# Kernel tuning notes

Hardware: AMD Instinct MI355X
Metric: run time of the kernel (lower is better)

## Reference

```python
import jax, jax.numpy as jnp
import numpy as np

CH = 256
CQK = CH // 8
B, H, W = 4, 64, 64


def setup_inputs() -> dict:
    key = jax.random.key(0)
    ks = jax.random.split(key, 8)
    s_qk = 1.0 / np.sqrt(CH)  # MSR init for 1x1 conv: std = 1/sqrt(fan_in)
    x = jax.random.normal(ks[0], (B, CH, H, W), dtype=jnp.float32)
    Wq = jax.random.normal(ks[1], (CQK, CH), dtype=jnp.float32) * s_qk
    bq = jnp.zeros((CQK,), dtype=jnp.float32)
    Wk = jax.random.normal(ks[2], (CQK, CH), dtype=jnp.float32) * s_qk
    bk = jnp.zeros((CQK,), dtype=jnp.float32)
    Wv = jax.random.normal(ks[3], (CH, CH), dtype=jnp.float32) * s_qk
    bv = jnp.zeros((CH,), dtype=jnp.float32)
    # NOTE: module inits gamma=0; use a nonzero value so the attention branch is active
    gamma = jnp.float32(0.5) * jnp.ones((1,), dtype=jnp.float32)
    return {"x": x, "Wq": Wq, "bq": bq, "Wk": Wk, "bk": bk, "Wv": Wv, "bv": bv, "gamma": gamma}


def reference(x, Wq, bq, Wk, bk, Wv, bv, gamma):
    b, c, h, w = x.shape
    n = h * w
    xf = x.reshape(b, c, n)  # [B, C, N]
    # 1x1 convs are per-pixel channel projections
    q = jnp.einsum('oc,bcn->bon', Wq, xf) + bq[:, None]  # [B, C/8, N]
    k = jnp.einsum('oc,bcn->bon', Wk, xf) + bk[:, None]  # [B, C/8, N]
    v = jnp.einsum('oc,bcn->bon', Wv, xf) + bv[:, None]  # [B, C, N]
    # scores[b, i, j] = q[:, i] . k[:, j]  (no scaling, as in source)
    att = jax.nn.softmax(jnp.einsum('bci,bcj->bij', q, k), axis=-1)  # [B, N, N]
    out = jnp.einsum('bcj,bij->bci', v, att).reshape(b, c, h, w)
    return x + gamma[0] * out
```

## Files before the change

### kernel.cpp

```cpp
#include <hip/hip_runtime.h>
#include <hip/hip_bf16.h>

typedef unsigned short u16;
typedef __attribute__((ext_vector_type(8))) __bf16 bf16x8;
typedef __attribute__((ext_vector_type(8))) unsigned short u16x8;
typedef __attribute__((ext_vector_type(4))) float f32x4;
typedef __attribute__((ext_vector_type(16))) float f32x16;
typedef __attribute__((ext_vector_type(4))) unsigned int u32x4;
typedef __attribute__((ext_vector_type(2))) unsigned int u32x2;

#define MFMA16(a, b, c) __builtin_amdgcn_mfma_f32_16x16x32_bf16((a), (b), (c), 0, 0, 0)
#define MFMA32(a, b, c) __builtin_amdgcn_mfma_f32_32x32x16_bf16((a), (b), (c), 0, 0, 0)

#define BN 4
#define CH 256
#define CQK 32
#define NPIX 4096

__device__ __forceinline__ u16 f2bf(float f) {
    __hip_bfloat16 h = __float2bfloat16(f);
    return *reinterpret_cast<u16*>(&h);
}

__device__ __forceinline__ unsigned pack2(float a, float b) {
    return (unsigned)f2bf(a) | ((unsigned)f2bf(b) << 16);
}

__device__ __forceinline__ unsigned packtr(float a, float b) {
    return (__float_as_uint(b) & 0xffff0000u) | (__float_as_uint(a) >> 16);
}

__device__ __forceinline__ float bf2f(u16 v) {
    return __uint_as_float(((unsigned)v) << 16);
}

__device__ __forceinline__ f32x16 zero16() {
    f32x16 z;
#pragma unroll
    for (int i = 0; i < 16; ++i) z[i] = 0.f;
    return z;
}

__device__ __forceinline__ int perm16(int k) {
    return (k & 3) | ((k & 4) << 1) | ((k & 8) >> 1);
}

__global__ void k_transpose(const float* __restrict__ x, u16* __restrict__ xt) {
    __shared__ float xs[64][65];
    int n0 = blockIdx.x * 64, c0 = blockIdx.y * 64, b = blockIdx.z;
    int t = threadIdx.x;
    const float* xp = x + ((size_t)(b * CH + c0)) * NPIX + n0;
#pragma unroll
    for (int it = 0; it < 16; ++it) {
        int idx = it * 256 + t;
        int cc = idx >> 6, nn = idx & 63;
        xs[cc][nn] = xp[(size_t)cc * NPIX + nn];
    }
    __syncthreads();
    u16* op = xt + ((size_t)(b * NPIX + n0)) * CH + c0;
#pragma unroll
    for (int it = 0; it < 16; ++it) {
        int idx = it * 256 + t;
        int nn = idx >> 6, cc = idx & 63;
        op[(size_t)nn * CH + cc] = f2bf(xs[cc][nn]);
    }
}

__global__ void k_wcvt(const float* __restrict__ Wq, const float* __restrict__ Wk,
                       const float* __restrict__ Wv, u16* __restrict__ Wbf) {
    int idx = blockIdx.x * 256 + threadIdx.x;
    int o = idx >> 8, c = idx & 255;
    float v;
    if (o < 32) v = Wq[o * 256 + c];
    else if (o < 64) v = Wk[(o - 32) * 256 + c];
    else v = Wv[(o - 64) * 256 + c];
    Wbf[idx] = f2bf(v);
}

__launch_bounds__(256, 1)
__global__ void k_proj(const u16* __restrict__ Wbf, const u16* __restrict__ xt,
                       const float* __restrict__ bq, const float* __restrict__ bk,
                       const float* __restrict__ bv,
                       u16* __restrict__ qb, u16* __restrict__ kb, u16* __restrict__ vb) {
    int b = blockIdx.y, n0 = blockIdx.x * 64;
    int t = threadIdx.x, w = t >> 6, l = t & 63;
    int lr = l & 15, lg = l >> 4;

    f32x4 acc[5][4];
#pragma unroll
    for (int s = 0; s < 5; ++s)
#pragma unroll
        for (int u = 0; u < 4; ++u) acc[s][u] = f32x4{0.f, 0.f, 0.f, 0.f};

    const u16* xtb = xt + ((size_t)(b * NPIX + n0)) * CH;

#pragma unroll
    for (int kk = 0; kk < 8; ++kk) {
        int kof = kk * 32 + lg * 8;
        bf16x8 af[5], bfr[4];
#pragma unroll
        for (int s = 0; s < 5; ++s) {
            int o = w * 16 + s * 64 + lr;
            af[s] = *reinterpret_cast<const bf16x8*>(Wbf + (size_t)o * 256 + kof);
        }
#pragma unroll
        for (int u = 0; u < 4; ++u) {
            int n = u * 16 + lr;
            bfr[u] = *reinterpret_cast<const bf16x8*>(xtb + (size_t)n * CH + kof);
        }
#pragma unroll
        for (int s = 0; s < 5; ++s)
#pragma unroll
            for (int u = 0; u < 4; ++u) acc[s][u] = MFMA16(af[s], bfr[u], acc[s][u]);
    }

    int lrp = perm16(lr);
#pragma unroll
    for (int s = 0; s < 5; ++s) {
        int o0 = w * 16 + s * 64;
#pragma unroll
        for (int r = 0; r < 4; ++r) {
            int o = o0 + lg * 4 + r;
            float bias = (o < 32) ? bq[o] : (o < 64) ? bk[o - 32] : bv[o - 64];
#pragma unroll
            for (int u = 0; u < 4; ++u) {
                float val = acc[s][u][r] + bias;
                u16 h = f2bf(val);
                if (o < 32) qb[((size_t)b * NPIX + n0 + u * 16 + lr) * CQK + o] = h;
                else if (o < 64) kb[((size_t)b * NPIX + n0 + u * 16 + lr) * CQK + (o - 32)] = h;
                else vb[((size_t)(b * CH + (o - 64))) * NPIX + n0 + u * 16 + lrp] = h;
            }
        }
    }
}

template <int NCHUNK>
__launch_bounds__(256, 2)
__global__ void k_attn5(const u16* __restrict__ qb, const u16* __restrict__ kb,
                        const u16* __restrict__ vb, const float* __restrict__ x,
                        const float* __restrict__ gamma,
                        u16* __restrict__ pacc, float* __restrict__ plsum,
                        float* __restrict__ out) {
    constexpr int JCH = NPIX / NCHUNK;
    constexpr int NT = JCH / 32;
    int it = blockIdx.x, s = blockIdx.y, b = blockIdx.z;
    int t = threadIdx.x, w = t >> 6, l = t & 63;
    int lr = l & 31, hi = l >> 5;
    int i0 = it * 128;
    int j0 = s * JCH;

    __shared__ u16 vlds[3][256][32];
    __shared__ float lsl[128];

    const u16* qrow = qb + ((size_t)b * NPIX + i0 + w * 32 + lr) * CQK;
    bf16x8 qf0 = *(const bf16x8*)(qrow + hi * 8);
    bf16x8 qf1 = *(const bf16x8*)(qrow + 16 + hi * 8);

    const u16* kbase = kb + (size_t)b * NPIX * CQK;
    const u16* vbase = vb + (size_t)(b * CH) * NPIX;

    f32x16 acc[8];
#pragma unroll
    for (int ct = 0; ct < 8; ++ct) acc[ct] = zero16();
    float lsum_p = 0.f;

    int srow = t >> 2, sslot = t & 3;
    int wslot = (sslot ^ (srow & 3)) * 8;
    bf16x8 vst[4];
    bf16x8 kc0, kc1;

    auto vload = [&](int tt) {
#pragma unroll
        for (int m = 0; m < 4; ++m)
            vst[m] = *(const bf16x8*)(vbase + (size_t)(64 * m + srow) * NPIX +
                                      j0 + tt * 32 + sslot * 8);
    };
    auto vwrite = [&](int buf) {
        u16* base = &vlds[buf][0][0];
#pragma unroll
        for (int m = 0; m < 4; ++m)
            *(bf16x8*)(base + (64 * m + srow) * 32 + wslot) = vst[m];
    };
    auto kload = [&](int tt) {
        const u16* kr = kbase + (size_t)(j0 + tt * 32 + lr) * CQK;
        kc0 = *(const bf16x8*)(kr + hi * 8);
        kc1 = *(const bf16x8*)(kr + 16 + hi * 8);
    };
    auto qkexp = [&](bf16x8 k0, bf16x8 k1, bf16x8& p0, bf16x8& p1) {
        f32x16 sf = MFMA32(k0, qf0, zero16());
        sf = MFMA32(k1, qf1, sf);
        float P[16];
#pragma unroll
        for (int e = 0; e < 16; ++e) {
            P[e] = __expf(sf[e] - 32.0f);
            lsum_p += P[e];
        }
        u32x4 a = {packtr(P[0], P[1]), packtr(P[2], P[3]),
                   packtr(P[4], P[5]), packtr(P[6], P[7])};
        u32x4 c = {packtr(P[8], P[9]), packtr(P[10], P[11]),
                   packtr(P[12], P[13]), packtr(P[14], P[15])};
        p0 = __builtin_bit_cast(bf16x8, a);
        p1 = __builtin_bit_cast(bf16x8, c);
    };
    auto pv = [&](int buf, bf16x8 p0, bf16x8 p1) {
        const u16* base = &vlds[buf][0][0];
#pragma unroll
        for (int ct = 0; ct < 8; ++ct) {
            int c = ct * 32 + lr;
            int sw = lr & 3;
            bf16x8 vf0 = *(const bf16x8*)(base + c * 32 + ((hi ^ sw) * 8));
            bf16x8 vf1 = *(const bf16x8*)(base + c * 32 + (((2 + hi) ^ sw) * 8));
            acc[ct] = MFMA32(p0, vf0, acc[ct]);
            acc[ct] = MFMA32(p1, vf1, acc[ct]);
        }
    };
    auto lds_barrier = [&]() {
        asm volatile("s_waitcnt lgkmcnt(0)" ::: "memory");
        __builtin_amdgcn_s_barrier();
    };

    bf16x8 paA0, paA1, paB0, paB1;
    vload(0);
    kload(0);
    vwrite(0);
    vload(1);
    lds_barrier();
    qkexp(kc0, kc1, paA0, paA1);
    if (1 < NT) kload(1);
    vwrite(1);
    if (2 < NT) vload(2);

    int bR = 0, bW = 2;
    for (int tt = 0; tt < NT; ++tt) {
        if (tt + 1 < NT) qkexp(kc0, kc1, paB0, paB1);
        if (tt + 2 < NT) kload(tt + 2);
        pv(bR, paA0, paA1);
        if (tt + 2 < NT) vwrite(bW);
        if (tt + 3 < NT) vload(tt + 3);
        lds_barrier();
        if (tt + 1 < NT) { paA0 = paB0; paA1 = paB1; }
        bR = (bR == 2) ? 0 : bR + 1;
        bW = (bW == 2) ? 0 : bW + 1;
    }

    lsum_p += __shfl_xor(lsum_p, 32);

    if constexpr (NCHUNK == 1) {
        float g = gamma[0];
        if (l < 32) lsl[w * 32 + l] = g / lsum_p;
        __syncthreads();
#pragma unroll
        for (int ct = 0; ct < 8; ++ct) {
            int c = ct * 32 + lr;
            const float* xp = x + ((size_t)(b * CH + c)) * NPIX + i0;
            float* op = out + ((size_t)(b * CH + c)) * NPIX + i0;
#pragma unroll
            for (int r = 0; r < 16; ++r) {
                int il = w * 32 + (r & 3) + 8 * (r >> 2) + 4 * hi;
                op[il] = xp[il] + acc[ct][r] * lsl[il];
            }
        }
    } else {
        size_t pbase = ((((size_t)s * BN + b) * 32 + it) * 256) * 128;
#pragma unroll
        for (int ct = 0; ct < 8; ++ct) {
            int c = ct * 32 + lr;
#pragma unroll
            for (int q = 0; q < 4; ++q) {
                int il0 = w * 32 + 8 * q + 4 * hi;
                u32x2 pr = {pack2(acc[ct][4 * q], acc[ct][4 * q + 1]),
                            pack2(acc[ct][4 * q + 2], acc[ct][4 * q + 3])};
                *(u32x2*)(pacc + pbase + (size_t)c * 128 + il0) = pr;
            }
        }
        if (l < 32)
            plsum[(((size_t)s * BN + b) * 32 + it) * 128 + w * 32 + l] = lsum_p;
    }
}

template <int NCHUNK>
__global__ void k_reduce(const u16* __restrict__ pacc, const float* __restrict__ plsum,
                         const float* __restrict__ x, const float* __restrict__ gamma,
                         float* __restrict__ out) {
    int cg = blockIdx.x, it = blockIdx.y, b = blockIdx.z;
    int t = threadIdx.x;
    int c0 = cg * 32;
    __shared__ float invl[128];

    if (t < 128) {
        float lt = 0.f;
#pragma unroll
        for (int s = 0; s < NCHUNK; ++s)
            lt += plsum[(((size_t)s * BN + b) * 32 + it) * 128 + t];
        invl[t] = gamma[0] / lt;
    }
    __syncthreads();

    const size_t chunk_stride = (size_t)BN * 32 * 256 * 128;
    size_t base = (((size_t)b * 32 + it) * 256 + c0) * 128;

#pragma unroll
    for (int k = 0; k < 2; ++k) {
        int v = k * 256 + t;
        int cl = v >> 4;
        int io = (v & 15) * 8;
        size_t off = base + (size_t)cl * 128 + io;
        f32x4 a0 = {0.f, 0.f, 0.f, 0.f}, a1 = a0;
#pragma unroll
        for (int s = 0; s < NCHUNK; ++s) {
            u16x8 p = *(const u16x8*)(pacc + (size_t)s * chunk_stride + off);
            a0[0] += bf2f(p[0]); a0[1] += bf2f(p[1]); a0[2] += bf2f(p[2]); a0[3] += bf2f(p[3]);
            a1[0] += bf2f(p[4]); a1[1] += bf2f(p[5]); a1[2] += bf2f(p[6]); a1[3] += bf2f(p[7]);
        }
        f32x4 i0v = *(const f32x4*)(&invl[io]);
        f32x4 i1v = *(const f32x4*)(&invl[io + 4]);
        size_t oi = ((size_t)(b * CH + c0 + cl)) * NPIX + it * 128 + io;
        f32x4 x0 = *(const f32x4*)(x + oi);
        f32x4 x1 = *(const f32x4*)(x + oi + 4);
        *(f32x4*)(out + oi) = x0 + a0 * i0v;
        *(f32x4*)(out + oi + 4) = x1 + a1 * i1v;
    }
}

extern "C" void kernel_launch(void* const* d_in, const int* in_sizes, int n_in,
                              void* d_out, int out_size, void* d_ws, size_t ws_size,
                              hipStream_t stream) {
    const float* x = (const float*)d_in[0];
    const float* Wq = (const float*)d_in[1];
    const float* bq = (const float*)d_in[2];
    const float* Wk = (const float*)d_in[3];
    const float* bk = (const float*)d_in[4];
    const float* Wv = (const float*)d_in[5];
    const float* bv = (const float*)d_in[6];
    const float* gamma = (const float*)d_in[7];
    float* out = (float*)d_out;

    char* ws = (char*)d_ws;
    u16* xt = (u16*)(ws);
    u16* Wbf = (u16*)(ws + 8388608);
    u16* qb = (u16*)(ws + 8388608 + 163840);
    u16* kb = (u16*)(ws + 8388608 + 163840 + 1048576);
    u16* vb = (u16*)(ws + 8388608 + 163840 + 2097152);
    const size_t base_end = 8388608 + 163840 + 2097152 + 8388608;
    u16* pacc = (u16*)(ws + base_end);

    hipLaunchKernelGGL(k_transpose, dim3(64, 4, 4), dim3(256), 0, stream, x, xt);
    hipLaunchKernelGGL(k_wcvt, dim3(320), dim3(256), 0, stream, Wq, Wk, Wv, Wbf);
    hipLaunchKernelGGL(k_proj, dim3(64, 4), dim3(256), 0, stream, Wbf, xt, bq, bk, bv, qb, kb, vb);

    const size_t pacc4 = (size_t)4 * BN * NPIX * CH * 2;
    const size_t pls4 = (size_t)4 * BN * NPIX * 4;
    const size_t pacc2 = pacc4 / 2, pls2 = pls4 / 2;

    if (ws_size >= base_end + pacc4 + pls4) {
        float* plsum = (float*)(ws + base_end + pacc4);
        hipLaunchKernelGGL(k_attn5<4>, dim3(32, 4, 4), dim3(256), 0, stream,
                           qb, kb, vb, x, gamma, pacc, plsum, out);
        hipLaunchKernelGGL(k_reduce<4>, dim3(8, 32, 4), dim3(256), 0, stream,
                           pacc, plsum, x, gamma, out);
    } else if (ws_size >= base_end + pacc2 + pls2) {
        float* plsum = (float*)(ws + base_end + pacc2);
        hipLaunchKernelGGL(k_attn5<2>, dim3(32, 2, 4), dim3(256), 0, stream,
                           qb, kb, vb, x, gamma, pacc, plsum, out);
        hipLaunchKernelGGL(k_reduce<2>, dim3(8, 32, 4), dim3(256), 0, stream,
                           pacc, plsum, x, gamma, out);
    } else {
        hipLaunchKernelGGL(k_attn5<1>, dim3(32, 1, 4), dim3(256), 0, stream,
                           qb, kb, vb, x, gamma, pacc, (float*)pacc, out);
    }
}
```

Measured before the change: 93.25 us.

## Split attention work across 8 waves by query and channel quarters

```diff
diff --git a/kernel.cpp b/kernel.cpp
--- a/kernel.cpp
+++ b/kernel.cpp
@@ -135,8 +135,8 @@
 }
 
 template <int NCHUNK>
-__launch_bounds__(256, 2)
-__global__ void k_attn5(const u16* __restrict__ qb, const u16* __restrict__ kb,
+__launch_bounds__(512, 2)
+__global__ void k_attn6(const u16* __restrict__ qb, const u16* __restrict__ kb,
                         const u16* __restrict__ vb, const float* __restrict__ x,
                         const float* __restrict__ gamma,
                         u16* __restrict__ pacc, float* __restrict__ plsum,
@@ -146,72 +146,85 @@
     int it = blockIdx.x, s = blockIdx.y, b = blockIdx.z;
     int t = threadIdx.x, w = t >> 6, l = t & 63;
     int lr = l & 31, hi = l >> 5;
+    int iq2 = w >> 2, ch4 = w & 3;
     int i0 = it * 128;
     int j0 = s * JCH;
 
     __shared__ u16 vlds[3][256][32];
     __shared__ float lsl[128];
 
-    const u16* qrow = qb + ((size_t)b * NPIX + i0 + w * 32 + lr) * CQK;
-    bf16x8 qf0 = *(const bf16x8*)(qrow + hi * 8);
-    bf16x8 qf1 = *(const bf16x8*)(qrow + 16 + hi * 8);
+    bf16x8 qf[2][2];
+#pragma unroll
+    for (int is = 0; is < 2; ++is) {
+        const u16* qrow = qb + ((size_t)b * NPIX + i0 + iq2 * 64 + is * 32 + lr) * CQK;
+        qf[is][0] = *(const bf16x8*)(qrow + hi * 8);
+        qf[is][1] = *(const bf16x8*)(qrow + 16 + hi * 8);
+    }
 
     const u16* kbase = kb + (size_t)b * NPIX * CQK;
     const u16* vbase = vb + (size_t)(b * CH) * NPIX;
 
-    f32x16 acc[8];
-#pragma unroll
-    for (int ct = 0; ct < 8; ++ct) acc[ct] = zero16();
-    float lsum_p = 0.f;
-
-    int srow = t >> 2, sslot = t & 3;
-    int wslot = (sslot ^ (srow & 3)) * 8;
-    bf16x8 vst[4];
+    f32x16 acc[2][2];
+#pragma unroll
+    for (int is = 0; is < 2; ++is)
+#pragma unroll
+        for (int ct = 0; ct < 2; ++ct) acc[is][ct] = zero16();
+    float lsum[2] = {0.f, 0.f};
+
+    int row0 = t >> 2, sslot = t & 3;
+    int wso = (sslot ^ (row0 & 3)) * 8;
+    bf16x8 vst[2];
     bf16x8 kc0, kc1;
 
     auto vload = [&](int tt) {
 #pragma unroll
-        for (int m = 0; m < 4; ++m)
-            vst[m] = *(const bf16x8*)(vbase + (size_t)(64 * m + srow) * NPIX +
+        for (int m = 0; m < 2; ++m)
+            vst[m] = *(const bf16x8*)(vbase + (size_t)(row0 + 128 * m) * NPIX +
                                       j0 + tt * 32 + sslot * 8);
     };
     auto vwrite = [&](int buf) {
         u16* base = &vlds[buf][0][0];
 #pragma unroll
-        for (int m = 0; m < 4; ++m)
-            *(bf16x8*)(base + (64 * m + srow) * 32 + wslot) = vst[m];
+        for (int m = 0; m < 2; ++m)
+            *(bf16x8*)(base + (row0 + 128 * m) * 32 + wso) = vst[m];
     };
     auto kload = [&](int tt) {
         const u16* kr = kbase + (size_t)(j0 + tt * 32 + lr) * CQK;
         kc0 = *(const bf16x8*)(kr + hi * 8);
         kc1 = *(const bf16x8*)(kr + 16 + hi * 8);
     };
-    auto qkexp = [&](bf16x8 k0, bf16x8 k1, bf16x8& p0, bf16x8& p1) {
-        f32x16 sf = MFMA32(k0, qf0, zero16());
-        sf = MFMA32(k1, qf1, sf);
-        float P[16];
-#pragma unroll
-        for (int e = 0; e < 16; ++e) {
-            P[e] = __expf(sf[e] - 32.0f);
-            lsum_p += P[e];
-        }
-        u32x4 a = {packtr(P[0], P[1]), packtr(P[2], P[3]),
-                   packtr(P[4], P[5]), packtr(P[6], P[7])};
-        u32x4 c = {packtr(P[8], P[9]), packtr(P[10], P[11]),
-                   packtr(P[12], P[13]), packtr(P[14], P[15])};
-        p0 = __builtin_bit_cast(bf16x8, a);
-        p1 = __builtin_bit_cast(bf16x8, c);
-    };
-    auto pv = [&](int buf, bf16x8 p0, bf16x8 p1) {
+    auto qkexp = [&](bf16x8 k0, bf16x8 k1, bf16x8 (&pa)[4]) {
+#pragma unroll
+        for (int is = 0; is < 2; ++is) {
+            f32x16 sf = MFMA32(k0, qf[is][0], zero16());
+            sf = MFMA32(k1, qf[is][1], sf);
+            float P[16];
+#pragma unroll
+            for (int e = 0; e < 16; ++e) {
+                P[e] = __expf(sf[e] - 32.0f);
+                lsum[is] += P[e];
+            }
+            u32x4 a = {packtr(P[0], P[1]), packtr(P[2], P[3]),
+                       packtr(P[4], P[5]), packtr(P[6], P[7])};
+            u32x4 c = {packtr(P[8], P[9]), packtr(P[10], P[11]),
+                       packtr(P[12], P[13]), packtr(P[14], P[15])};
+            pa[is * 2] = __builtin_bit_cast(bf16x8, a);
+            pa[is * 2 + 1] = __builtin_bit_cast(bf16x8, c);
+        }
+    };
+    auto pv = [&](int buf, bf16x8 (&pa)[4]) {
         const u16* base = &vlds[buf][0][0];
 #pragma unroll
-        for (int ct = 0; ct < 8; ++ct) {
-            int c = ct * 32 + lr;
-            int sw = lr & 3;
+        for (int ct = 0; ct < 2; ++ct) {
+            int c = ch4 * 64 + ct * 32 + lr;
+            int sw = c & 3;
             bf16x8 vf0 = *(const bf16x8*)(base + c * 32 + ((hi ^ sw) * 8));
             bf16x8 vf1 = *(const bf16x8*)(base + c * 32 + (((2 + hi) ^ sw) * 8));
-            acc[ct] = MFMA32(p0, vf0, acc[ct]);
-            acc[ct] = MFMA32(p1, vf1, acc[ct]);
+#pragma unroll
+            for (int is = 0; is < 2; ++is) {
+                acc[is][ct] = MFMA32(pa[is * 2], vf0, acc[is][ct]);
+                acc[is][ct] = MFMA32(pa[is * 2 + 1], vf1, acc[is][ct]);
+            }
         }
     };
     auto lds_barrier = [&]() {
@@ -219,62 +232,76 @@
         __builtin_amdgcn_s_barrier();
     };
 
-    bf16x8 paA0, paA1, paB0, paB1;
+    bf16x8 paA[4], paB[4];
     vload(0);
     kload(0);
     vwrite(0);
     vload(1);
     lds_barrier();
-    qkexp(kc0, kc1, paA0, paA1);
+    qkexp(kc0, kc1, paA);
     if (1 < NT) kload(1);
     vwrite(1);
     if (2 < NT) vload(2);
 
     int bR = 0, bW = 2;
     for (int tt = 0; tt < NT; ++tt) {
-        if (tt + 1 < NT) qkexp(kc0, kc1, paB0, paB1);
+        if (tt + 1 < NT) qkexp(kc0, kc1, paB);
         if (tt + 2 < NT) kload(tt + 2);
-        pv(bR, paA0, paA1);
+        pv(bR, paA);
         if (tt + 2 < NT) vwrite(bW);
         if (tt + 3 < NT) vload(tt + 3);
         lds_barrier();
-        if (tt + 1 < NT) { paA0 = paB0; paA1 = paB1; }
+        if (tt + 1 < NT) {
+#pragma unroll
+            for (int e = 0; e < 4; ++e) paA[e] = paB[e];
+        }
         bR = (bR == 2) ? 0 : bR + 1;
         bW = (bW == 2) ? 0 : bW + 1;
     }
 
-    lsum_p += __shfl_xor(lsum_p, 32);
+    lsum[0] += __shfl_xor(lsum[0], 32);
+    lsum[1] += __shfl_xor(lsum[1], 32);
 
     if constexpr (NCHUNK == 1) {
         float g = gamma[0];
-        if (l < 32) lsl[w * 32 + l] = g / lsum_p;
+        if (ch4 == 0 && l < 32) {
+            lsl[iq2 * 64 + l] = g / lsum[0];
+            lsl[iq2 * 64 + 32 + l] = g / lsum[1];
+        }
         __syncthreads();
 #pragma unroll
-        for (int ct = 0; ct < 8; ++ct) {
-            int c = ct * 32 + lr;
-            const float* xp = x + ((size_t)(b * CH + c)) * NPIX + i0;
-            float* op = out + ((size_t)(b * CH + c)) * NPIX + i0;
-#pragma unroll
-            for (int r = 0; r < 16; ++r) {
-                int il = w * 32 + (r & 3) + 8 * (r >> 2) + 4 * hi;
-                op[il] = xp[il] + acc[ct][r] * lsl[il];
-            }
-        }
+        for (int is = 0; is < 2; ++is)
+#pragma unroll
+            for (int ct = 0; ct < 2; ++ct) {
+                int c = ch4 * 64 + ct * 32 + lr;
+                const float* xp = x + ((size_t)(b * CH + c)) * NPIX + i0;
+                float* op = out + ((size_t)(b * CH + c)) * NPIX + i0;
+#pragma unroll
+                for (int r = 0; r < 16; ++r) {
+                    int il = iq2 * 64 + is * 32 + (r & 3) + 8 * (r >> 2) + 4 * hi;
+                    op[il] = xp[il] + acc[is][ct][r] * lsl[il];
+                }
+            }
     } else {
         size_t pbase = ((((size_t)s * BN + b) * 32 + it) * 256) * 128;
 #pragma unroll
-        for (int ct = 0; ct < 8; ++ct) {
-            int c = ct * 32 + lr;
-#pragma unroll
-            for (int q = 0; q < 4; ++q) {
-                int il0 = w * 32 + 8 * q + 4 * hi;
-                u32x2 pr = {pack2(acc[ct][4 * q], acc[ct][4 * q + 1]),
-                            pack2(acc[ct][4 * q + 2], acc[ct][4 * q + 3])};
-                *(u32x2*)(pacc + pbase + (size_t)c * 128 + il0) = pr;
-            }
-        }
-        if (l < 32)
-            plsum[(((size_t)s * BN + b) * 32 + it) * 128 + w * 32 + l] = lsum_p;
+        for (int is = 0; is < 2; ++is)
+#pragma unroll
+            for (int ct = 0; ct < 2; ++ct) {
+                int c = ch4 * 64 + ct * 32 + lr;
+#pragma unroll
+                for (int q = 0; q < 4; ++q) {
+                    int il0 = iq2 * 64 + is * 32 + 8 * q + 4 * hi;
+                    u32x2 pr = {pack2(acc[is][ct][4 * q], acc[is][ct][4 * q + 1]),
+                                pack2(acc[is][ct][4 * q + 2], acc[is][ct][4 * q + 3])};
+                    *(u32x2*)(pacc + pbase + (size_t)c * 128 + il0) = pr;
+                }
+            }
+        if (ch4 == 0 && l < 32) {
+            size_t lb = (((size_t)s * BN + b) * 32 + it) * 128 + iq2 * 64;
+            plsum[lb + l] = lsum[0];
+            plsum[lb + 32 + l] = lsum[1];
+        }
     }
 }
 
@@ -348,24 +375,17 @@
     hipLaunchKernelGGL(k_wcvt, dim3(320), dim3(256), 0, stream, Wq, Wk, Wv, Wbf);
     hipLaunchKernelGGL(k_proj, dim3(64, 4), dim3(256), 0, stream, Wbf, xt, bq, bk, bv, qb, kb, vb);
 
-    const size_t pacc4 = (size_t)4 * BN * NPIX * CH * 2;
-    const size_t pls4 = (size_t)4 * BN * NPIX * 4;
-    const size_t pacc2 = pacc4 / 2, pls2 = pls4 / 2;
-
-    if (ws_size >= base_end + pacc4 + pls4) {
-        float* plsum = (float*)(ws + base_end + pacc4);
-        hipLaunchKernelGGL(k_attn5<4>, dim3(32, 4, 4), dim3(256), 0, stream,
-                           qb, kb, vb, x, gamma, pacc, plsum, out);
-        hipLaunchKernelGGL(k_reduce<4>, dim3(8, 32, 4), dim3(256), 0, stream,
-                           pacc, plsum, x, gamma, out);
-    } else if (ws_size >= base_end + pacc2 + pls2) {
+    const size_t pacc2 = (size_t)2 * BN * NPIX * CH * 2;
+    const size_t pls2 = (size_t)2 * BN * NPIX * 4;
+
+    if (ws_size >= base_end + pacc2 + pls2) {
         float* plsum = (float*)(ws + base_end + pacc2);
-        hipLaunchKernelGGL(k_attn5<2>, dim3(32, 2, 4), dim3(256), 0, stream,
+        hipLaunchKernelGGL(k_attn6<2>, dim3(32, 2, 4), dim3(512), 0, stream,
                            qb, kb, vb, x, gamma, pacc, plsum, out);
         hipLaunchKernelGGL(k_reduce<2>, dim3(8, 32, 4), dim3(256), 0, stream,
                            pacc, plsum, x, gamma, out);
     } else {
-        hipLaunchKernelGGL(k_attn5<1>, dim3(32, 1, 4), dim3(256), 0, stream,
+        hipLaunchKernelGGL(k_attn6<1>, dim3(32, 1, 4), dim3(512), 0, stream,
                            qb, kb, vb, x, gamma, pacc, (float*)pacc, out);
     }
 }
```

Measured after the change: 112.4 us. +20.6%, slower.
